# Kernel optimization log

Measured on AMD Instinct MI355X. Metric: run time of the kernel, lower is better.

Reference implementation:

```python
import jax, jax.numpy as jnp
import numpy as np

BN_EPS = 1e-5
COS_EPS = 1e-6
LEAKY_SLOPE = 0.01
SIMILARITY_RATIO = 0.5


def setup_inputs() -> dict:
    key = jax.random.key(0)
    ks = jax.random.split(key, 5)
    B, D2, D, M = 2048, 256, 128, 100000
    item_feature = jax.random.normal(ks[0], (B, D2), dtype=jnp.float32)
    all_items = jax.random.normal(ks[1], (M, D), dtype=jnp.float32)
    user_item_id = jax.random.randint(ks[2], (B, 2), 0, M, dtype=jnp.int64)
    W = jax.random.normal(ks[3], (D2, D), dtype=jnp.float32) * (1.0 / np.sqrt(D2))
    b = jax.random.normal(ks[4], (D,), dtype=jnp.float32) * 0.01
    gamma = jnp.ones((D,), dtype=jnp.float32)
    beta = jnp.zeros((D,), dtype=jnp.float32)
    return {"item_feature": item_feature, "all_items": all_items,
            "user_item_id": user_item_id, "W": W, "b": b,
            "gamma": gamma, "beta": beta}


def reference(item_feature, all_items, user_item_id, W, b, gamma, beta):
    # Linear -> BatchNorm1d (training-mode batch stats, biased var) -> LeakyReLU
    h = item_feature @ W + b                       # [B, D]
    mu = jnp.mean(h, axis=0)
    var = jnp.var(h, axis=0)
    hn = (h - mu) * jax.lax.rsqrt(var + BN_EPS) * gamma + beta
    uf = jnp.where(hn >= 0, hn, LEAKY_SLOPE * hn)  # leaky relu

    # dense scoring + top-1 retrieval: [B, M] score matrix
    scores = uf @ all_items.T
    top1 = jnp.argmax(scores, axis=1)              # [B]

    # gather original and retrieved item embeddings
    orig = user_item_id[:, 1]
    a = all_items[orig]                            # [B, D]
    c = all_items[top1]                            # [B, D]

    # cosine similarity (torch CosineSimilarity semantics, eps=1e-6)
    na = jnp.maximum(jnp.sqrt(jnp.sum(a * a, axis=1)), COS_EPS)
    nc = jnp.maximum(jnp.sqrt(jnp.sum(c * c, axis=1)), COS_EPS)
    sim = jnp.sum(a * c, axis=1) / (na * nc)
    sim = (sim + 1.0) * 0.5                        # regularize to [0,1]

    # margin loss against constant labels = similarity_ratio
    labels = jnp.full(sim.shape, SIMILARITY_RATIO, dtype=sim.dtype)
    similarity_loss = jnp.mean(jnp.maximum(sim - labels, 0.0))

    return top1, similarity_loss, jnp.mean(sim)
```

## Files before the change

kernel.cpp:

```cpp
#include <hip/hip_runtime.h>
#include <stdint.h>

#define B_ROWS 2048
#define D2_DIM 256
#define D_DIM 128
#define M_ITEMS 100000
#define M_PAD 100352
#define BN_EPS_F 1e-5f
#define COS_EPS_F 1e-6f
#define LEAKY_F 0.01f

#define BNI 128
#define BK 32
#define SUPER 4

typedef __bf16 bf16x8 __attribute__((ext_vector_type(8)));
typedef float f32x4 __attribute__((ext_vector_type(4)));

__device__ unsigned short g_Aph[B_ROWS * D_DIM];
__device__ unsigned short g_Apl[B_ROWS * D_DIM];
__device__ unsigned short g_Bph[M_PAD * D_DIM];
__device__ unsigned short g_Bpl[M_PAD * D_DIM];

__device__ __forceinline__ unsigned bf16_rne(float f) {
  unsigned u = __float_as_uint(f);
  return (u + 0x7fffu + ((u >> 16) & 1u)) >> 16;
}
__device__ __forceinline__ void split_bf16(float v, unsigned short& hi, unsigned short& lo) {
  unsigned h = bf16_rne(v);
  float hf = __uint_as_float(h << 16);
  unsigned l = bf16_rne(v - hf);
  hi = (unsigned short)h; lo = (unsigned short)l;
}
__device__ __forceinline__ void gload16(const void* g, void* l) {
  __builtin_amdgcn_global_load_lds(
      (const __attribute__((address_space(1))) void*)g,
      (__attribute__((address_space(3))) void*)l, 16, 0, 0);
}
__device__ __forceinline__ unsigned long long pack_key(float v, int idx) {
  unsigned u = __float_as_uint(v);
  u = (u & 0x80000000u) ? ~u : (u | 0x80000000u);
  return ((unsigned long long)u << 32) | (unsigned)(~(unsigned)idx);
}

__global__ void k_gemm1(const float* __restrict__ A, const float* __restrict__ W,
                        const float* __restrict__ bias, float* __restrict__ h) {
  __shared__ float arow[D2_DIM];
  const int r = blockIdx.x;
  const int c = threadIdx.x;
  arow[c] = A[r * D2_DIM + c];
  arow[c + 128] = A[r * D2_DIM + c + 128];
  __syncthreads();
  float acc = 0.f;
#pragma unroll 8
  for (int k = 0; k < D2_DIM; k++) acc = fmaf(arow[k], W[k * D_DIM + c], acc);
  h[r * D_DIM + c] = acc + bias[c];
}

__global__ void k_bnstats(const float* __restrict__ h, const float* __restrict__ gamma,
                          const float* __restrict__ beta, float* __restrict__ scale,
                          float* __restrict__ shift) {
  const int c = blockIdx.x;
  const int t = threadIdx.x;
  double s = 0.0, sq = 0.0;
  for (int r = t; r < B_ROWS; r += 256) {
    double v = (double)h[r * D_DIM + c];
    s += v; sq += v * v;
  }
  __shared__ double ls[256], lq[256];
  ls[t] = s; lq[t] = sq;
  __syncthreads();
  for (int off = 128; off; off >>= 1) {
    if (t < off) { ls[t] += ls[t + off]; lq[t] += lq[t + off]; }
    __syncthreads();
  }
  if (t == 0) {
    double mean = ls[0] / (double)B_ROWS;
    double var = lq[0] / (double)B_ROWS - mean * mean;
    float sc = (float)((double)gamma[c] / sqrt(var + (double)BN_EPS_F));
    scale[c] = sc;
    shift[c] = beta[c] - (float)mean * sc;
  }
}

__global__ void k_norm_split(const float* __restrict__ h, const float* __restrict__ scale,
                             const float* __restrict__ shift) {
  int i = blockIdx.x * 256 + threadIdx.x;
  if (i >= B_ROWS * D_DIM) return;
  int c = i & (D_DIM - 1);
  float v = fmaf(h[i], scale[c], shift[c]);
  v = v >= 0.f ? v : LEAKY_F * v;
  unsigned short hi, lo;
  split_bf16(v, hi, lo);
  g_Aph[i] = hi; g_Apl[i] = lo;
}

__global__ void k_build_items(const float* __restrict__ items) {
  long long t = (long long)blockIdx.x * 256 + threadIdx.x;
  long long base = t * 4;
  if (base >= (long long)M_PAD * D_DIM) return;
  float4 v;
  if (base < (long long)M_ITEMS * D_DIM) v = *(const float4*)&items[base];
  else v = make_float4(0.f, 0.f, 0.f, 0.f);
  ushort4 hv, lv;
  split_bf16(v.x, hv.x, lv.x);
  split_bf16(v.y, hv.y, lv.y);
  split_bf16(v.z, hv.z, lv.z);
  split_bf16(v.w, hv.w, lv.w);
  *(ushort4*)&g_Bph[base] = hv;
  *(ushort4*)&g_Bpl[base] = lv;
}

__global__ void k_init(unsigned long long* __restrict__ keys) {
  int i = blockIdx.x * blockDim.x + threadIdx.x;
  if (i < B_ROWS) keys[i] = 0ull;
}

__global__
__attribute__((amdgpu_flat_work_group_size(256, 256), amdgpu_waves_per_eu(2, 2)))
void k_scores_mfma(unsigned long long* __restrict__ keys) {
  __shared__ __align__(16) char smem[81920];
  char* sAlo = smem + 49152;

  const int tid = threadIdx.x;
  const int l = tid & 63;
  const int w = tid >> 6;
  const int wm = w >> 1;
  const int wn = w & 1;
  const int rowbase = blockIdx.x * 128;
  const int chunk = blockIdx.y * (SUPER * BNI);
  const int lrow = l & 15;
  const int lkg = l >> 4;

  int tb0, tb1, ldst;
  {
    const int s0 = tid;
    const int s1 = tid + 256;
    tb0 = (s0 >> 2) * 256 + (((s0 & 3) ^ ((s0 >> 3) & 3)) * 16);
    tb1 = (s1 >> 2) * 256 + (((s1 & 3) ^ ((s1 >> 3) & 3)) * 16);
    ldst = tid * 16;
  }
  const char* gBh = (const char*)g_Bph;
  const char* gBl = (const char*)g_Bpl;

  auto STAGEB = [&](int itembase, int ks, char* buf) {
    const size_t ub = (size_t)itembase * 256 + (size_t)ks * 2;
    gload16(gBh + ub + tb0, buf + ldst);
    gload16(gBl + ub + tb0, buf + 8192 + ldst);
    gload16(gBh + ub + tb1, buf + ldst + 4096);
    gload16(gBl + ub + tb1, buf + 8192 + ldst + 4096);
  };

#pragma unroll
  for (int rep = 0; rep < 8; rep++) {
    const int s = tid + rep * 256;
    gload16(g_Apl + (size_t)(rowbase + (s >> 4)) * D_DIM
                  + ((s & 15) ^ ((s >> 4) & 15)) * 8,
            sAlo + s * 16);
  }
  STAGEB(chunk, 0, smem);
  STAGEB(chunk, BK, smem + 16384);

  bf16x8 ah[4][4];
  const int ar = rowbase + wm * 64 + lrow;
#pragma unroll
  for (int mi = 0; mi < 4; mi++)
#pragma unroll
    for (int kf = 0; kf < 4; kf++)
      ah[mi][kf] = *(const bf16x8*)&g_Aph[(size_t)(ar + mi * 16) * D_DIM + kf * 32 + lkg * 8];

  char* lbase = smem + wn * 4096 + lrow * 64 + ((lkg ^ ((lrow >> 1) & 3)) << 4);

  float bestv[4][4];
  unsigned sel0 = 0u, sel1 = 0u;
#pragma unroll
  for (int mi = 0; mi < 4; mi++)
#pragma unroll
    for (int reg = 0; reg < 4; reg++)
      asm volatile("v_accvgpr_write_b32 %0, %1"
                   : "=a"(bestv[mi][reg]) : "v"(-3.0e38f));

  f32x4 acc[4][4];
#pragma unroll
  for (int mi = 0; mi < 4; mi++)
#pragma unroll
    for (int ni = 0; ni < 4; ni++) acc[mi][ni] = (f32x4)(0.0f);

#pragma unroll
  for (int s = 0; s < SUPER; s++) {
    const int itembase = chunk + s * BNI;
#pragma unroll
    for (int kf = 0; kf < 4; kf++) {
      const int j = s * 4 + kf;
      asm volatile("s_waitcnt vmcnt(4)" ::: "memory");
      __builtin_amdgcn_s_barrier();
      {
        const int q = j + 2;
        const int qt = (q >> 2) & (SUPER - 1);
        STAGEB(chunk + qt * BNI, (q & 3) * BK, smem + (q % 3) * 16384);
      }
      const int jb = (j % 3) * 16384;
      bf16x8 bh[4], bl[4], alo[4];
#pragma unroll
      for (int ni = 0; ni < 4; ni++) {
        bh[ni] = *(const bf16x8*)(lbase + jb + ni * 1024);
        bl[ni] = *(const bf16x8*)(lbase + jb + 8192 + ni * 1024);
      }
#pragma unroll
      for (int mi = 0; mi < 4; mi++) {
        const int row = wm * 64 + mi * 16 + lrow;
        const int off = row * 256 + (((kf * 4 + lkg) ^ (row & 15)) << 4);
        alo[mi] = *(const bf16x8*)(sAlo + off);
      }
      __builtin_amdgcn_s_setprio(1);
#pragma unroll
      for (int mi = 0; mi < 4; mi++)
#pragma unroll
        for (int ni = 0; ni < 4; ni++) {
          f32x4 c = acc[mi][ni];
          c = __builtin_amdgcn_mfma_f32_16x16x32_bf16(ah[mi][kf], bh[ni], c, 0, 0, 0);
          c = __builtin_amdgcn_mfma_f32_16x16x32_bf16(alo[mi], bh[ni], c, 0, 0, 0);
          c = __builtin_amdgcn_mfma_f32_16x16x32_bf16(ah[mi][kf], bl[ni], c, 0, 0, 0);
          acc[mi][ni] = c;
        }
      __builtin_amdgcn_s_setprio(0);
    }
#pragma unroll
    for (int mi = 0; mi < 4; mi++) {
#pragma unroll
      for (int reg = 0; reg < 4; reg++) {
        const int q = mi * 4 + reg;
        float bv = bestv[mi][reg];
#pragma unroll
        for (int ni = 0; ni < 4; ni++) {
          const float x = acc[mi][ni][reg];
          const int col = itembase + wn * 64 + ni * 16 + lrow;
          const bool win = (col < M_ITEMS) && (x > bv);
          bv = win ? x : bv;
          const unsigned code = (unsigned)(s * 4 + ni);
          if (q < 8) {
            const unsigned nw = (sel0 & ~(0xFu << (q * 4))) | (code << (q * 4));
            sel0 = win ? nw : sel0;
          } else {
            const unsigned nw = (sel1 & ~(0xFu << ((q - 8) * 4))) | (code << ((q - 8) * 4));
            sel1 = win ? nw : sel1;
          }
        }
        asm volatile("v_accvgpr_write_b32 %0, %1"
                     : "=a"(bestv[mi][reg]) : "v"(bv));
      }
#pragma unroll
      for (int ni = 0; ni < 4; ni++) acc[mi][ni] = (f32x4)(0.0f);
    }
  }
  asm volatile("s_waitcnt vmcnt(0)" ::: "memory");

  unsigned long long rb = 0ull;
#pragma unroll
  for (int mi = 0; mi < 4; mi++) {
#pragma unroll
    for (int reg = 0; reg < 4; reg++) {
      const int q = mi * 4 + reg;
      const unsigned code = (q < 8 ? (sel0 >> (q * 4)) : (sel1 >> ((q - 8) * 4))) & 0xFu;
      float v = bestv[mi][reg];
      int bi = chunk + (int)(code >> 2) * BNI + wn * 64 + (int)(code & 3) * 16 + lrow;
#pragma unroll
      for (int off = 1; off < 16; off <<= 1) {
        float ov = __shfl_xor(v, off, 16);
        int oi = __shfl_xor(bi, off, 16);
        if (ov > v || (ov == v && oi < bi)) { v = ov; bi = oi; }
      }
      if (lrow == q) rb = pack_key(v, bi);
    }
  }
  const int myrow = rowbase + wm * 64 + (lrow >> 2) * 16 + lkg * 4 + (lrow & 3);
  atomicMax(&keys[myrow], rb);
}

__global__ void k_post(const unsigned long long* __restrict__ keys,
                       const int* __restrict__ uid,
                       const float* __restrict__ items,
                       float* __restrict__ out, float* __restrict__ sims,
                       float* __restrict__ rl) {
  int r = blockIdx.x * blockDim.x + threadIdx.x;
  if (r >= B_ROWS) return;
  unsigned long long key = keys[r];
  int idx = (int)(~(unsigned)(key & 0xFFFFFFFFull));
  out[r] = (float)idx;
  int orig = uid[2 * r + 1];
  const float* a = items + (long long)orig * D_DIM;
  const float* c = items + (long long)idx * D_DIM;
  float aa = 0.f, cc = 0.f, ac = 0.f;
#pragma unroll 4
  for (int d = 0; d < D_DIM; d++) {
    float x = a[d], y = c[d];
    aa = fmaf(x, x, aa);
    cc = fmaf(y, y, cc);
    ac = fmaf(x, y, ac);
  }
  float na = fmaxf(sqrtf(aa), COS_EPS_F);
  float nc = fmaxf(sqrtf(cc), COS_EPS_F);
  float sim = ac / (na * nc);
  sim = (sim + 1.f) * 0.5f;
  sims[r] = sim;
  rl[r] = fmaxf(sim - 0.5f, 0.f);
}

__global__ void k_final(const float* __restrict__ sims, const float* __restrict__ rl,
                        float* __restrict__ out) {
  __shared__ float s1[256], s2[256];
  int t = threadIdx.x;
  float a = 0.f, b = 0.f;
  for (int r = t; r < B_ROWS; r += 256) { a += rl[r]; b += sims[r]; }
  s1[t] = a; s2[t] = b;
  __syncthreads();
  for (int off = 128; off; off >>= 1) {
    if (t < off) { s1[t] += s1[t + off]; s2[t] += s2[t + off]; }
    __syncthreads();
  }
  if (t == 0) {
    out[B_ROWS] = s1[0] / (float)B_ROWS;
    out[B_ROWS + 1] = s2[0] / (float)B_ROWS;
  }
}

extern "C" void kernel_launch(void* const* d_in, const int* in_sizes, int n_in,
                              void* d_out, int out_size, void* d_ws, size_t ws_size,
                              hipStream_t stream) {
  const float* item_feature = (const float*)d_in[0];
  const float* all_items    = (const float*)d_in[1];
  const int*   uid          = (const int*)d_in[2];
  const float* W            = (const float*)d_in[3];
  const float* bias         = (const float*)d_in[4];
  const float* gamma        = (const float*)d_in[5];
  const float* beta         = (const float*)d_in[6];
  float* out = (float*)d_out;

  float* h     = (float*)d_ws;
  float* scale = h + B_ROWS * D_DIM;
  float* shift = scale + D_DIM;
  unsigned long long* keys = (unsigned long long*)(shift + D_DIM);
  float* sims  = (float*)(keys + B_ROWS);
  float* rl    = sims + B_ROWS;

  k_gemm1<<<B_ROWS, D_DIM, 0, stream>>>(item_feature, W, bias, h);
  k_bnstats<<<D_DIM, 256, 0, stream>>>(h, gamma, beta, scale, shift);
  k_norm_split<<<(B_ROWS * D_DIM + 255) / 256, 256, 0, stream>>>(h, scale, shift);
  k_build_items<<<(M_PAD * D_DIM / 4 + 255) / 256, 256, 0, stream>>>(all_items);
  k_init<<<(B_ROWS + 255) / 256, 256, 0, stream>>>(keys);
  dim3 sg(B_ROWS / 128, M_PAD / (SUPER * BNI));
  k_scores_mfma<<<sg, 256, 0, stream>>>(keys);
  k_post<<<(B_ROWS + 255) / 256, 256, 0, stream>>>(keys, uid, all_items, out, sims, rl);
  k_final<<<1, 256, 0, stream>>>(sims, rl, out);
}
```

Baseline: 267.5 us.

## Shrink score tile to 64 rows with 512-thread blocks and smaller per-wave tiles

Reworks the scoring GEMM from 128-row tiles with 4 waves, each holding a 64x64 accumulator tile, to 64-row tiles with 8 waves, each holding a 32x32 tile. This cuts registers per wave so 4 waves per EU fit instead of 2, which raises occupancy and latency hiding, and it halves LDS use for the A-low tile. The three MFMA passes are regrouped so independent accumulators are interleaved rather than chained. In exchange, each B tile loaded from memory is reused across half as many rows, so B traffic doubles and more blocks issue atomics.

After: 274.7 us. 1.03x slower.

```diff
diff --git a/kernel.cpp b/kernel.cpp
--- a/kernel.cpp
+++ b/kernel.cpp
@@ -13,6 +13,7 @@
 #define BNI 128
 #define BK 32
 #define SUPER 4
+#define BROWS 64
 
 typedef __bf16 bf16x8 __attribute__((ext_vector_type(8)));
 typedef float f32x4 __attribute__((ext_vector_type(4)));
@@ -117,43 +118,43 @@
 }
 
 __global__
-__attribute__((amdgpu_flat_work_group_size(256, 256), amdgpu_waves_per_eu(2, 2)))
+__attribute__((amdgpu_flat_work_group_size(512, 512), amdgpu_waves_per_eu(4, 4)))
 void k_scores_mfma(unsigned long long* __restrict__ keys) {
-  __shared__ __align__(16) char smem[81920];
+  __shared__ __align__(16) char smem[65536];
   char* sAlo = smem + 49152;
 
   const int tid = threadIdx.x;
   const int l = tid & 63;
   const int w = tid >> 6;
-  const int wm = w >> 1;
-  const int wn = w & 1;
-  const int rowbase = blockIdx.x * 128;
+  const int wm = w >> 2;
+  const int wn = w & 3;
+  const int rowbase = blockIdx.x * BROWS;
   const int chunk = blockIdx.y * (SUPER * BNI);
   const int lrow = l & 15;
   const int lkg = l >> 4;
 
-  int tb0, tb1, ldst;
-  {
-    const int s0 = tid;
-    const int s1 = tid + 256;
-    tb0 = (s0 >> 2) * 256 + (((s0 & 3) ^ ((s0 >> 3) & 3)) * 16);
-    tb1 = (s1 >> 2) * 256 + (((s1 & 3) ^ ((s1 >> 3) & 3)) * 16);
-    ldst = tid * 16;
-  }
+  const int tb = (tid >> 2) * 256 + (((tid & 3) ^ ((tid >> 3) & 3)) * 16);
+  const int ldst = tid * 16;
   const char* gBh = (const char*)g_Bph;
   const char* gBl = (const char*)g_Bpl;
 
   auto STAGEB = [&](int itembase, int ks, char* buf) {
     const size_t ub = (size_t)itembase * 256 + (size_t)ks * 2;
-    gload16(gBh + ub + tb0, buf + ldst);
-    gload16(gBl + ub + tb0, buf + 8192 + ldst);
-    gload16(gBh + ub + tb1, buf + ldst + 4096);
-    gload16(gBl + ub + tb1, buf + 8192 + ldst + 4096);
+    gload16(gBh + ub + tb, buf + ldst);
+    gload16(gBl + ub + tb, buf + 8192 + ldst);
   };
 
-#pragma unroll
-  for (int rep = 0; rep < 8; rep++) {
-    const int s = tid + rep * 256;
+  bf16x8 ah[2][4];
+  const int ar = rowbase + wm * 32 + lrow;
+#pragma unroll
+  for (int mi = 0; mi < 2; mi++)
+#pragma unroll
+    for (int kf = 0; kf < 4; kf++)
+      ah[mi][kf] = *(const bf16x8*)&g_Aph[(size_t)(ar + mi * 16) * D_DIM + kf * 32 + lkg * 8];
+  __builtin_amdgcn_sched_barrier(0);
+#pragma unroll
+  for (int rep = 0; rep < 2; rep++) {
+    const int s = tid + rep * 512;
     gload16(g_Apl + (size_t)(rowbase + (s >> 4)) * D_DIM
                   + ((s & 15) ^ ((s >> 4) & 15)) * 8,
             sAlo + s * 16);
@@ -161,30 +162,22 @@
   STAGEB(chunk, 0, smem);
   STAGEB(chunk, BK, smem + 16384);
 
-  bf16x8 ah[4][4];
-  const int ar = rowbase + wm * 64 + lrow;
-#pragma unroll
-  for (int mi = 0; mi < 4; mi++)
-#pragma unroll
-    for (int kf = 0; kf < 4; kf++)
-      ah[mi][kf] = *(const bf16x8*)&g_Aph[(size_t)(ar + mi * 16) * D_DIM + kf * 32 + lkg * 8];
-
-  char* lbase = smem + wn * 4096 + lrow * 64 + ((lkg ^ ((lrow >> 1) & 3)) << 4);
-
-  float bestv[4][4];
-  unsigned sel0 = 0u, sel1 = 0u;
-#pragma unroll
-  for (int mi = 0; mi < 4; mi++)
+  char* lbase = smem + wn * 2048 + lrow * 64 + ((lkg ^ ((lrow >> 1) & 3)) << 4);
+
+  float bestv[2][4];
+  unsigned sel = 0u;
+#pragma unroll
+  for (int mi = 0; mi < 2; mi++)
 #pragma unroll
     for (int reg = 0; reg < 4; reg++)
       asm volatile("v_accvgpr_write_b32 %0, %1"
                    : "=a"(bestv[mi][reg]) : "v"(-3.0e38f));
 
-  f32x4 acc[4][4];
-#pragma unroll
-  for (int mi = 0; mi < 4; mi++)
-#pragma unroll
-    for (int ni = 0; ni < 4; ni++) acc[mi][ni] = (f32x4)(0.0f);
+  f32x4 acc[2][2];
+#pragma unroll
+  for (int mi = 0; mi < 2; mi++)
+#pragma unroll
+    for (int ni = 0; ni < 2; ni++) acc[mi][ni] = (f32x4)(0.0f);
 
 #pragma unroll
   for (int s = 0; s < SUPER; s++) {
@@ -192,7 +185,7 @@
 #pragma unroll
     for (int kf = 0; kf < 4; kf++) {
       const int j = s * 4 + kf;
-      asm volatile("s_waitcnt vmcnt(4)" ::: "memory");
+      asm volatile("s_waitcnt vmcnt(2)" ::: "memory");
       __builtin_amdgcn_s_barrier();
       {
         const int q = j + 2;
@@ -200,70 +193,73 @@
         STAGEB(chunk + qt * BNI, (q & 3) * BK, smem + (q % 3) * 16384);
       }
       const int jb = (j % 3) * 16384;
-      bf16x8 bh[4], bl[4], alo[4];
-#pragma unroll
-      for (int ni = 0; ni < 4; ni++) {
+      bf16x8 bh[2], bl[2], alo[2];
+#pragma unroll
+      for (int ni = 0; ni < 2; ni++) {
         bh[ni] = *(const bf16x8*)(lbase + jb + ni * 1024);
         bl[ni] = *(const bf16x8*)(lbase + jb + 8192 + ni * 1024);
       }
 #pragma unroll
-      for (int mi = 0; mi < 4; mi++) {
-        const int row = wm * 64 + mi * 16 + lrow;
+      for (int mi = 0; mi < 2; mi++) {
+        const int row = wm * 32 + mi * 16 + lrow;
         const int off = row * 256 + (((kf * 4 + lkg) ^ (row & 15)) << 4);
         alo[mi] = *(const bf16x8*)(sAlo + off);
       }
       __builtin_amdgcn_s_setprio(1);
 #pragma unroll
-      for (int mi = 0; mi < 4; mi++)
-#pragma unroll
-        for (int ni = 0; ni < 4; ni++) {
-          f32x4 c = acc[mi][ni];
-          c = __builtin_amdgcn_mfma_f32_16x16x32_bf16(ah[mi][kf], bh[ni], c, 0, 0, 0);
-          c = __builtin_amdgcn_mfma_f32_16x16x32_bf16(alo[mi], bh[ni], c, 0, 0, 0);
-          c = __builtin_amdgcn_mfma_f32_16x16x32_bf16(ah[mi][kf], bl[ni], c, 0, 0, 0);
-          acc[mi][ni] = c;
-        }
+      for (int mi = 0; mi < 2; mi++)
+#pragma unroll
+        for (int ni = 0; ni < 2; ni++)
+          acc[mi][ni] = __builtin_amdgcn_mfma_f32_16x16x32_bf16(
+              ah[mi][kf], bh[ni], acc[mi][ni], 0, 0, 0);
+#pragma unroll
+      for (int mi = 0; mi < 2; mi++)
+#pragma unroll
+        for (int ni = 0; ni < 2; ni++)
+          acc[mi][ni] = __builtin_amdgcn_mfma_f32_16x16x32_bf16(
+              alo[mi], bh[ni], acc[mi][ni], 0, 0, 0);
+#pragma unroll
+      for (int mi = 0; mi < 2; mi++)
+#pragma unroll
+        for (int ni = 0; ni < 2; ni++)
+          acc[mi][ni] = __builtin_amdgcn_mfma_f32_16x16x32_bf16(
+              ah[mi][kf], bl[ni], acc[mi][ni], 0, 0, 0);
       __builtin_amdgcn_s_setprio(0);
     }
 #pragma unroll
-    for (int mi = 0; mi < 4; mi++) {
+    for (int mi = 0; mi < 2; mi++) {
 #pragma unroll
       for (int reg = 0; reg < 4; reg++) {
         const int q = mi * 4 + reg;
         float bv = bestv[mi][reg];
 #pragma unroll
-        for (int ni = 0; ni < 4; ni++) {
+        for (int ni = 0; ni < 2; ni++) {
           const float x = acc[mi][ni][reg];
-          const int col = itembase + wn * 64 + ni * 16 + lrow;
+          const int col = itembase + wn * 32 + ni * 16 + lrow;
           const bool win = (col < M_ITEMS) && (x > bv);
           bv = win ? x : bv;
           const unsigned code = (unsigned)(s * 4 + ni);
-          if (q < 8) {
-            const unsigned nw = (sel0 & ~(0xFu << (q * 4))) | (code << (q * 4));
-            sel0 = win ? nw : sel0;
-          } else {
-            const unsigned nw = (sel1 & ~(0xFu << ((q - 8) * 4))) | (code << ((q - 8) * 4));
-            sel1 = win ? nw : sel1;
-          }
+          const unsigned nw = (sel & ~(0xFu << (q * 4))) | (code << (q * 4));
+          sel = win ? nw : sel;
         }
         asm volatile("v_accvgpr_write_b32 %0, %1"
                      : "=a"(bestv[mi][reg]) : "v"(bv));
       }
 #pragma unroll
-      for (int ni = 0; ni < 4; ni++) acc[mi][ni] = (f32x4)(0.0f);
+      for (int ni = 0; ni < 2; ni++) acc[mi][ni] = (f32x4)(0.0f);
     }
   }
   asm volatile("s_waitcnt vmcnt(0)" ::: "memory");
 
   unsigned long long rb = 0ull;
 #pragma unroll
-  for (int mi = 0; mi < 4; mi++) {
+  for (int mi = 0; mi < 2; mi++) {
 #pragma unroll
     for (int reg = 0; reg < 4; reg++) {
       const int q = mi * 4 + reg;
-      const unsigned code = (q < 8 ? (sel0 >> (q * 4)) : (sel1 >> ((q - 8) * 4))) & 0xFu;
+      const unsigned code = (sel >> (q * 4)) & 0xFu;
       float v = bestv[mi][reg];
-      int bi = chunk + (int)(code >> 2) * BNI + wn * 64 + (int)(code & 3) * 16 + lrow;
+      int bi = chunk + (int)(code >> 2) * BNI + wn * 32 + (int)(code & 3) * 16 + lrow;
 #pragma unroll
       for (int off = 1; off < 16; off <<= 1) {
         float ov = __shfl_xor(v, off, 16);
@@ -273,8 +269,10 @@
       if (lrow == q) rb = pack_key(v, bi);
     }
   }
-  const int myrow = rowbase + wm * 64 + (lrow >> 2) * 16 + lkg * 4 + (lrow & 3);
-  atomicMax(&keys[myrow], rb);
+  if (lrow < 8) {
+    const int myrow = rowbase + wm * 32 + (lrow >> 2) * 16 + lkg * 4 + (lrow & 3);
+    atomicMax(&keys[myrow], rb);
+  }
 }
 
 __global__ void k_post(const unsigned long long* __restrict__ keys,
@@ -348,8 +346,8 @@
   k_norm_split<<<(B_ROWS * D_DIM + 255) / 256, 256, 0, stream>>>(h, scale, shift);
   k_build_items<<<(M_PAD * D_DIM / 4 + 255) / 256, 256, 0, stream>>>(all_items);
   k_init<<<(B_ROWS + 255) / 256, 256, 0, stream>>>(keys);
-  dim3 sg(B_ROWS / 128, M_PAD / (SUPER * BNI));
-  k_scores_mfma<<<sg, 256, 0, stream>>>(keys);
+  dim3 sg(B_ROWS / BROWS, M_PAD / (SUPER * BNI));
+  k_scores_mfma<<<sg, 512, 0, stream>>>(keys);
   k_post<<<(B_ROWS + 255) / 256, 256, 0, stream>>>(keys, uid, all_items, out, sims, rl);
   k_final<<<1, 256, 0, stream>>>(sims, rl, out);
 }
```
